# Optimization experiments

Hardware: AMD Instinct MI355X
Metric: run time of the kernel (lower is better)

## Reference

```python
import jax, jax.numpy as jnp
import numpy as np

B, T, C = 4, 2048, 1024
N_HEAD = 16
HEAD = C // N_HEAD  # 64


def _rope_tables(T, dim, base=10000.0):
    inv_freq = 1.0 / (base ** (jnp.arange(0, dim, 2, dtype=jnp.float32) / dim))
    t = jnp.arange(T, dtype=jnp.float32)
    freqs = jnp.einsum('i,j->ij', t, inv_freq)           # [T, dim/2]
    emb = jnp.concatenate([freqs, freqs], axis=-1)        # [T, dim]
    return jnp.cos(emb), jnp.sin(emb)                     # each [T, dim]


def _rotate_half(x):
    x1, x2 = x[..., : x.shape[-1] // 2], x[..., x.shape[-1] // 2:]
    return jnp.concatenate([-x2, x1], axis=-1)


def setup_inputs() -> dict:
    key = jax.random.key(0)
    ks = jax.random.split(key, 4)
    x = jax.random.normal(ks[0], (B, T, C), dtype=jnp.float32)
    w_attn = jax.random.normal(ks[1], (C, 3 * C), dtype=jnp.float32) * (1.0 / np.sqrt(C))
    b_attn = jnp.zeros((3 * C,), dtype=jnp.float32)
    w_proj = jax.random.normal(ks[2], (C, C), dtype=jnp.float32) * (1.0 / np.sqrt(C))
    b_proj = jnp.zeros((C,), dtype=jnp.float32)
    return {"x": x, "w_attn": w_attn, "b_attn": b_attn, "w_proj": w_proj, "b_proj": b_proj}


def reference(x, w_attn, b_attn, w_proj, b_proj):
    Bx, Tx, Cx = x.shape
    qkv = x @ w_attn + b_attn                             # [B,T,3C]
    q, k, v = jnp.split(qkv, 3, axis=-1)
    # [B,T,C] -> [B,H,T,hd]
    def to_heads(t):
        return t.reshape(Bx, Tx, N_HEAD, HEAD).transpose(0, 2, 1, 3)
    q, k, v = to_heads(q), to_heads(k), to_heads(v)
    cos, sin = _rope_tables(Tx, HEAD)                     # [T,hd]
    cos = cos[None, None, :, :]
    sin = sin[None, None, :, :]
    q = q * cos + _rotate_half(q) * sin
    k = k * cos + _rotate_half(k) * sin
    scale = 1.0 / np.sqrt(HEAD)
    att = jnp.einsum('bhqd,bhkd->bhqk', q, k) * scale     # [B,H,T,T]
    causal = jnp.tril(jnp.ones((Tx, Tx), dtype=bool))
    att = jnp.where(causal[None, None], att, -jnp.inf)
    att = jax.nn.softmax(att, axis=-1)
    y = jnp.einsum('bhqk,bhkd->bhqd', att, v)             # [B,H,T,hd]
    y = y.transpose(0, 2, 1, 3).reshape(Bx, Tx, Cx)
    return y @ w_proj + b_proj
```

## Files before the change

### kernel.cpp

```cpp
#include <hip/hip_runtime.h>

#define B_  4
#define T_  2048
#define C_  1024
#define NH_ 16
#define HD_ 64
#define BT_ (B_*T_)
#define N3C (3*C_)

typedef _Float16 f16;
typedef _Float16 half8 __attribute__((ext_vector_type(8)));
typedef _Float16 half4 __attribute__((ext_vector_type(4)));
typedef _Float16 half2v __attribute__((ext_vector_type(2)));
typedef float f32x4 __attribute__((ext_vector_type(4)));

__device__ __forceinline__ void gld16(const f16* g, f16* l) {
  __builtin_amdgcn_global_load_lds(
      (const __attribute__((address_space(1))) unsigned int*)g,
      (__attribute__((address_space(3))) unsigned int*)l, 16, 0, 0);
}

__device__ __forceinline__ float fast_exp2(float x) {
#if __has_builtin(__builtin_amdgcn_exp2f)
  return __builtin_amdgcn_exp2f(x);
#else
  return exp2f(x);
#endif
}

__device__ __forceinline__ half2v cvt_pk_f16(float a, float b) {
#if __has_builtin(__builtin_amdgcn_cvt_pkrtz)
  return __builtin_bit_cast(half2v, __builtin_amdgcn_cvt_pkrtz(a, b));
#else
  half2v r; r[0] = (f16)a; r[1] = (f16)b; return r;
#endif
}

__global__ __launch_bounds__(256) void prep(
    const float* __restrict__ X, f16* __restrict__ X16,
    const float* __restrict__ Wa, f16* __restrict__ Wta,
    const float* __restrict__ Wp, f16* __restrict__ Wtp,
    float2* __restrict__ cs)
{
  __shared__ float Ls[64][65];
  const int tid = threadIdx.x;
  const int blk = blockIdx.x;
  if (blk < 4096) {
    const int i = blk * 256 + tid;
    const float4 a = ((const float4*)X)[i * 2];
    const float4 b = ((const float4*)X)[i * 2 + 1];
    half8 hx;
    hx[0] = (f16)a.x; hx[1] = (f16)a.y; hx[2] = (f16)a.z; hx[3] = (f16)a.w;
    hx[4] = (f16)b.x; hx[5] = (f16)b.y; hx[6] = (f16)b.z; hx[7] = (f16)b.w;
    ((half8*)X16)[i] = hx;
    return;
  }
  if (blk >= 5120) {
    const int i = (blk - 5120) * 256 + tid;
    const int f = i & 31, t = i >> 5;
    const float inv = expf(-(2.0f * (float)f / 64.0f) * 9.210340371976184f);
    float sn, cn;
    sincosf((float)t * inv, &sn, &cn);
    cs[i] = make_float2(cn, sn);
    return;
  }
  const float* W; f16* Wt; int N, i2;
  if (blk < 4864) { W = Wa; Wt = Wta; N = N3C; i2 = blk - 4096; }
  else            { W = Wp; Wt = Wtp; N = C_;  i2 = blk - 4864; }
  const int nblk = N >> 6;
  const int n0 = (i2 % nblk) * 64, k0 = (i2 / nblk) * 64;
#pragma unroll
  for (int j = 0; j < 4; ++j) {
    const int idx = j * 256 + tid;
    const int r = idx >> 4, c = (idx & 15) * 4;
    const float4 w = *(const float4*)(W + (size_t)(k0 + r) * N + n0 + c);
    Ls[r][c + 0] = w.x; Ls[r][c + 1] = w.y; Ls[r][c + 2] = w.z; Ls[r][c + 3] = w.w;
  }
  __syncthreads();
#pragma unroll
  for (int j = 0; j < 2; ++j) {
    const int idx = j * 256 + tid;
    const int r = idx >> 3, c = (idx & 7) * 8;
    half8 hw;
#pragma unroll
    for (int u = 0; u < 8; ++u) hw[u] = (f16)Ls[c + u][r];
    *(half8*)(Wt + (size_t)(n0 + r) * C_ + k0 + c) = hw;
  }
}

__global__ __launch_bounds__(256) void gemm_qkv(
    const f16* __restrict__ A, const f16* __restrict__ Bt,
    const float* __restrict__ bias, const float2* __restrict__ cs,
    f16* __restrict__ Qo, f16* __restrict__ Ko, f16* __restrict__ Vt_g)
{
  __shared__ f16 S[16384];
  f16* As = S;
  f16* Bs = S + 8192;
  const int tid  = threadIdx.x;
  const int row0 = blockIdx.y * 128;
  const int col0 = blockIdx.x * 128;
  const int wave = tid >> 6, lane = tid & 63;
  const int l = lane & 15, quad = lane >> 4;
  const int wm = wave >> 1, wn = wave & 1;
  const int sr = tid >> 3;
  const int scs = ((tid & 7) ^ (sr & 7)) * 8;
  const int lq7 = l & 7;

  f32x4 acc[4][4];
#pragma unroll
  for (int mi = 0; mi < 4; ++mi)
#pragma unroll
    for (int ni = 0; ni < 4; ++ni) acc[mi][ni] = (f32x4)0.0f;

  for (int k0 = 0; k0 < C_; k0 += 64) {
    __syncthreads();
#pragma unroll
    for (int p = 0; p < 4; ++p) {
      const int r = p * 32 + sr;
      gld16(A  + (size_t)(row0 + r) * C_ + k0 + scs, &As[p * 2048 + tid * 8]);
      gld16(Bt + (size_t)(col0 + r) * C_ + k0 + scs, &Bs[p * 2048 + tid * 8]);
    }
    __syncthreads();

#pragma unroll
    for (int s = 0; s < 2; ++s) {
      half8 af[4], bf[4];
#pragma unroll
      for (int mi = 0; mi < 4; ++mi)
        af[mi] = *(const half8*)&As[(wm * 64 + mi * 16 + l) * 64 + ((((s << 2) | quad) ^ lq7) << 3)];
#pragma unroll
      for (int ni = 0; ni < 4; ++ni)
        bf[ni] = *(const half8*)&Bs[(wn * 64 + ni * 16 + l) * 64 + ((((s << 2) | quad) ^ lq7) << 3)];
#pragma unroll
      for (int mi = 0; mi < 4; ++mi)
#pragma unroll
        for (int ni = 0; ni < 4; ++ni)
          acc[mi][ni] = __builtin_amdgcn_mfma_f32_16x16x32_f16(af[mi], bf[ni], acc[mi][ni], 0, 0, 0);
    }
  }

  const int region = col0 >> 10;
  const int colw = col0 + wn * 64;
  const int bloc  = row0 >> 11;
  const int tbase = row0 & (T_ - 1);
  if (region < 2) {
    f16* dst = (region == 0) ? Qo : Ko;
    const float qs = (region == 0) ? 0.18033688f : 1.0f;
    __syncthreads();
#pragma unroll
    for (int mi = 0; mi < 4; ++mi) {
#pragma unroll
      for (int r = 0; r < 4; ++r) {
        const int t = wm * 64 + mi * 16 + quad * 4 + r;
        const int swz = ((t >> 2) & 3) << 3;
        const float2* csrow = cs + (tbase + t) * 32;
#pragma unroll
        for (int ni = 0; ni < 2; ++ni) {
          const int d = ni * 16 + l;
          const float2 c2 = csrow[d];
          const float x1 = acc[mi][ni][r]     + bias[colw + d];
          const float x2 = acc[mi][ni + 2][r] + bias[colw + d + 32];
          S[wn * 8192 + t * 64 + (d ^ swz)]        = (f16)((x1 * c2.x - x2 * c2.y) * qs);
          S[wn * 8192 + t * 64 + ((d + 32) ^ swz)] = (f16)((x2 * c2.x + x1 * c2.y) * qs);
        }
      }
    }
    __syncthreads();
#pragma unroll
    for (int j = 0; j < 8; ++j) {
      const int flat = j * 256 + tid;
      const int wnn  = flat >> 10;
      const int rem  = flat & 1023;
      const int t    = rem >> 3;
      const int d8   = rem & 7;
      const int swz  = (t >> 2) & 3;
      const half8 v  = *(const half8*)&S[wnn * 8192 + t * 64 + ((d8 ^ swz) << 3)];
      const int hh   = ((col0 + wnn * 64) & 1023) >> 6;
      *(half8*)(dst + ((size_t)(bloc * NH_ + hh) * T_ + tbase + t) * HD_ + d8 * 8) = v;
    }
  } else {
    __syncthreads();
#pragma unroll
    for (int mi = 0; mi < 4; ++mi) {
      const int t_loc = wm * 64 + mi * 16 + quad * 4;
#pragma unroll
      for (int ni = 0; ni < 4; ++ni) {
        const int d = ni * 16 + l;
        const float bs = bias[colw + d];
        half4 o;
#pragma unroll
        for (int r = 0; r < 4; ++r) o[r] = (f16)(acc[mi][ni][r] + bs);
        const int ts = t_loc ^ ((d & 15) << 3);
        *(half4*)&S[wn * 8192 + d * 128 + ts] = o;
      }
    }
    __syncthreads();
#pragma unroll
    for (int j = 0; j < 8; ++j) {
      const int flat = j * 256 + tid;
      const int buf  = flat >> 10;
      const int rem  = flat & 1023;
      const int d    = rem >> 4;
      const int tt   = (rem & 15) << 3;
      const half8 v  = *(const half8*)&S[buf * 8192 + d * 128 + (tt ^ ((d & 15) << 3))];
      const int hh   = ((col0 + buf * 64) & 1023) >> 6;
      *(half8*)(Vt_g + ((size_t)((bloc * NH_ + hh) * HD_ + d)) * T_ + tbase + tt) = v;
    }
  }
}

__global__ __launch_bounds__(256) void attn_mfma(
    const f16* __restrict__ Qg, const f16* __restrict__ Kg,
    const f16* __restrict__ Vt_g, f16* __restrict__ Y)
{
  __shared__ f16 Ks[2][64 * 64];
  __shared__ f16 Vt[2][64 * 64];
  const int tid  = threadIdx.x;
  const int w    = (blockIdx.x & 7) * 128 + (blockIdx.x >> 3);
  const int bh   = w >> 4;
  const int pr   = w & 15;
  const int b    = bh >> 4, h = bh & 15;
  const int wave = tid >> 6, lane = tid & 63;
  const int l    = lane & 15, quad = lane >> 4;
  const int lq7  = l & 7;
  const int r0   = tid >> 3, cc = tid & 7;

  const f16* kbase  = Kg   + (size_t)bh * T_ * HD_;
  const f16* vtbase = Vt_g + (size_t)bh * HD_ * T_;

  const int qts[2] = { 31 - pr, pr };

#pragma unroll 1
  for (int pass = 0; pass < 2; ++pass) {
    const int qt   = qts[pass];
    const int nkt  = qt + 1;
    const int qrow = qt * 64 + wave * 16 + l;

    half8 qf[2];
    {
      const f16* qp = Qg + ((size_t)bh * T_ + qrow) * HD_;
      qf[0] = *(const half8*)(qp + quad * 8);
      qf[1] = *(const half8*)(qp + 32 + quad * 8);
    }

    f32x4 O[4];
#pragma unroll
    for (int mi = 0; mi < 4; ++mi) O[mi] = (f32x4)0.0f;
    float l_run = 0.f;
    const f32x4 zz = (f32x4)0.0f;

    half8 hk[2], hv[2];
#pragma unroll
    for (int i = 0; i < 2; ++i) {
      const int r = i * 32 + r0;
      hk[i] = *(const half8*)(kbase + (size_t)r * HD_ + cc * 8);
      hv[i] = *(const half8*)(vtbase + (size_t)r * T_ + cc * 8);
    }

    if (pass == 1) __syncthreads();

    for (int kt = 0; kt < nkt; ++kt) {
      f16* KsB = Ks[kt & 1];
      f16* VtB = Vt[kt & 1];
#pragma unroll
      for (int i = 0; i < 2; ++i) {
        const int r = i * 32 + r0;
        const int cst = ((cc ^ (r & 7)) << 3);
        *(half8*)&KsB[r * 64 + cst] = hk[i];
        *(half8*)&VtB[r * 64 + cst] = hv[i];
      }
      __syncthreads();
      if (kt + 1 < nkt) {
#pragma unroll
        for (int i = 0; i < 2; ++i) {
          const int r = i * 32 + r0;
          hk[i] = *(const half8*)(kbase + (size_t)((kt + 1) * 64 + r) * HD_ + cc * 8);
          hv[i] = *(const half8*)(vtbase + (size_t)r * T_ + (kt + 1) * 64 + cc * 8);
        }
      }

      f32x4 St[4];
#pragma unroll
      for (int st = 0; st < 4; ++st) {
        const int row = st * 16 + l;
        const half8 af0 = *(const half8*)&KsB[row * 64 + (((quad) ^ lq7) << 3)];
        St[st] = __builtin_amdgcn_mfma_f32_16x16x32_f16(af0, qf[0], zz, 0, 0, 0);
        const half8 af1 = *(const half8*)&KsB[row * 64 + (((4 | quad) ^ lq7) << 3)];
        St[st] = __builtin_amdgcn_mfma_f32_16x16x32_f16(af1, qf[1], St[st], 0, 0, 0);
      }

      const bool domask = (kt == qt);
      const int k0 = kt * 64;
      half4 pf[4];
      float psum = 0.f;
#pragma unroll
      for (int st = 0; st < 4; ++st) {
        float pv[4];
#pragma unroll
        for (int r = 0; r < 4; ++r) {
          float x = St[st][r];
          if (domask) {
            const int key = k0 + st * 16 + quad * 4 + r;
            if (key > qrow) x = -1e9f;
          }
          const float ev = fast_exp2(x);
          pv[r] = ev;
          psum += ev;
        }
        const half2v lo = cvt_pk_f16(pv[0], pv[1]);
        const half2v hi = cvt_pk_f16(pv[2], pv[3]);
        pf[st][0] = lo[0]; pf[st][1] = lo[1];
        pf[st][2] = hi[0]; pf[st][3] = hi[1];
      }
      l_run += psum;

#pragma unroll
      for (int mi = 0; mi < 4; ++mi) {
        const int row = mi * 16 + l;
#pragma unroll
        for (int ki = 0; ki < 4; ++ki) {
          const int kch = (ki << 1) | (quad >> 1);
          const half4 vf = *(const half4*)&VtB[row * 64 + ((kch ^ lq7) << 3) + ((quad & 1) << 2)];
          O[mi] = __builtin_amdgcn_mfma_f32_16x16x16f16(vf, pf[ki], O[mi], 0, 0, 0);
        }
      }
    }

    float lt = l_run;
    lt += __shfl_xor(lt, 16);
    lt += __shfl_xor(lt, 32);
    const float inv = 1.0f / lt;
    f16* yp = Y + ((size_t)(b * T_) + qrow) * C_ + h * 64;
#pragma unroll
    for (int mi = 0; mi < 4; ++mi) {
      half4 o;
      o[0] = (f16)(O[mi][0] * inv); o[1] = (f16)(O[mi][1] * inv);
      o[2] = (f16)(O[mi][2] * inv); o[3] = (f16)(O[mi][3] * inv);
      *(half4*)(yp + mi * 16 + quad * 4) = o;
    }
  }
}

__global__ __launch_bounds__(256) void gemm_proj(
    const f16* __restrict__ A, const f16* __restrict__ Bt,
    const float* __restrict__ bias, float* __restrict__ Out)
{
  __shared__ f16 As[128 * 64];
  __shared__ f16 Bs[64 * 64];
  const int tid  = threadIdx.x;
  const int row0 = blockIdx.y * 128;
  const int col0 = blockIdx.x * 64;
  const int wave = tid >> 6, lane = tid & 63;
  const int l = lane & 15, quad = lane >> 4;
  const int wm = wave >> 1, wn = wave & 1;
  const int sr = tid >> 3;
  const int scs = ((tid & 7) ^ (sr & 7)) * 8;
  const int lq7 = l & 7;

  f32x4 acc[4][2];
#pragma unroll
  for (int mi = 0; mi < 4; ++mi)
#pragma unroll
    for (int ni = 0; ni < 2; ++ni) acc[mi][ni] = (f32x4)0.0f;

  for (int k0 = 0; k0 < C_; k0 += 64) {
    __syncthreads();
#pragma unroll
    for (int p = 0; p < 4; ++p) {
      const int r = p * 32 + sr;
      gld16(A + (size_t)(row0 + r) * C_ + k0 + scs, &As[p * 2048 + tid * 8]);
    }
#pragma unroll
    for (int p = 0; p < 2; ++p) {
      const int r = p * 32 + sr;
      gld16(Bt + (size_t)(col0 + r) * C_ + k0 + scs, &Bs[p * 2048 + tid * 8]);
    }
    __syncthreads();

#pragma unroll
    for (int s = 0; s < 2; ++s) {
      half8 af[4], bf[2];
#pragma unroll
      for (int mi = 0; mi < 4; ++mi)
        af[mi] = *(const half8*)&As[(wm * 64 + mi * 16 + l) * 64 + ((((s << 2) | quad) ^ lq7) << 3)];
#pragma unroll
      for (int ni = 0; ni < 2; ++ni)
        bf[ni] = *(const half8*)&Bs[(wn * 32 + ni * 16 + l) * 64 + ((((s << 2) | quad) ^ lq7) << 3)];
#pragma unroll
      for (int mi = 0; mi < 4; ++mi)
#pragma unroll
        for (int ni = 0; ni < 2; ++ni)
          acc[mi][ni] = __builtin_amdgcn_mfma_f32_16x16x32_f16(af[mi], bf[ni], acc[mi][ni], 0, 0, 0);
    }
  }

#pragma unroll
  for (int mi = 0; mi < 4; ++mi) {
#pragma unroll
    for (int ni = 0; ni < 2; ++ni) {
#pragma unroll
      for (int r = 0; r < 4; ++r) {
        const int gm = row0 + wm * 64 + mi * 16 + quad * 4 + r;
        const int n  = col0 + wn * 32 + ni * 16 + l;
        Out[(size_t)gm * C_ + n] = acc[mi][ni][r] + bias[n];
      }
    }
  }
}

extern "C" void kernel_launch(void* const* d_in, const int* in_sizes, int n_in,
                              void* d_out, int out_size, void* d_ws, size_t ws_size,
                              hipStream_t stream) {
  const float* x      = (const float*)d_in[0];
  const float* w_attn = (const float*)d_in[1];
  const float* b_attn = (const float*)d_in[2];
  const float* w_proj = (const float*)d_in[3];
  const float* b_proj = (const float*)d_in[4];
  float* out = (float*)d_out;

  const size_t elems = (size_t)BT_ * C_;
  f16* x16 = (f16*)d_ws;
  f16* wta = x16 + elems;
  f16* wtp = wta + (size_t)N3C * C_;
  f16* q   = wtp + (size_t)C_ * C_;
  f16* k   = q + elems;
  f16* vt  = k + elems;
  f16* y   = vt + elems;
  float2* cs = (float2*)(y + elems);

  prep<<<dim3(5376), 256, 0, stream>>>(x, x16, w_attn, wta, w_proj, wtp, cs);
  gemm_qkv<<<dim3(N3C / 128, BT_ / 128), 256, 0, stream>>>(x16, wta, b_attn, cs, q, k, vt);
  attn_mfma<<<dim3(1024), 256, 0, stream>>>(q, k, vt, y);
  gemm_proj<<<dim3(C_ / 64, BT_ / 128), 256, 0, stream>>>(y, wtp, b_proj, out);
}
```

Measured before the change: 259.3 us.

## Fuse x fp32-to-fp16 conversion into QKV GEMM and widen proj tile

The separate prep pass that converted x to fp16 is removed. The QKV GEMM now loads fp32 x directly, converts it in registers and writes it to shared memory, which saves one full-activation write and read. In exchange those A loads become synchronous register loads rather than async global-to-LDS loads, and each 128-column block re-reads the fp32 rows. The projection GEMM tile also widens from 128x64 to 128x128, giving more reuse per block but half as many blocks.

Result: slower. 275.2 us (+6.1%).

```diff
diff --git a/kernel.cpp b/kernel.cpp
--- a/kernel.cpp
+++ b/kernel.cpp
@@ -37,7 +37,6 @@
 }
 
 __global__ __launch_bounds__(256) void prep(
-    const float* __restrict__ X, f16* __restrict__ X16,
     const float* __restrict__ Wa, f16* __restrict__ Wta,
     const float* __restrict__ Wp, f16* __restrict__ Wtp,
     float2* __restrict__ cs)
@@ -45,18 +44,8 @@
   __shared__ float Ls[64][65];
   const int tid = threadIdx.x;
   const int blk = blockIdx.x;
-  if (blk < 4096) {
-    const int i = blk * 256 + tid;
-    const float4 a = ((const float4*)X)[i * 2];
-    const float4 b = ((const float4*)X)[i * 2 + 1];
-    half8 hx;
-    hx[0] = (f16)a.x; hx[1] = (f16)a.y; hx[2] = (f16)a.z; hx[3] = (f16)a.w;
-    hx[4] = (f16)b.x; hx[5] = (f16)b.y; hx[6] = (f16)b.z; hx[7] = (f16)b.w;
-    ((half8*)X16)[i] = hx;
-    return;
-  }
-  if (blk >= 5120) {
-    const int i = (blk - 5120) * 256 + tid;
+  if (blk >= 1024) {
+    const int i = (blk - 1024) * 256 + tid;
     const int f = i & 31, t = i >> 5;
     const float inv = expf(-(2.0f * (float)f / 64.0f) * 9.210340371976184f);
     float sn, cn;
@@ -65,8 +54,8 @@
     return;
   }
   const float* W; f16* Wt; int N, i2;
-  if (blk < 4864) { W = Wa; Wt = Wta; N = N3C; i2 = blk - 4096; }
-  else            { W = Wp; Wt = Wtp; N = C_;  i2 = blk - 4864; }
+  if (blk < 768) { W = Wa; Wt = Wta; N = N3C; i2 = blk; }
+  else           { W = Wp; Wt = Wtp; N = C_;  i2 = blk - 768; }
   const int nblk = N >> 6;
   const int n0 = (i2 % nblk) * 64, k0 = (i2 / nblk) * 64;
 #pragma unroll
@@ -89,7 +78,7 @@
 }
 
 __global__ __launch_bounds__(256) void gemm_qkv(
-    const f16* __restrict__ A, const f16* __restrict__ Bt,
+    const float* __restrict__ X, const f16* __restrict__ Bt,
     const float* __restrict__ bias, const float2* __restrict__ cs,
     f16* __restrict__ Qo, f16* __restrict__ Ko, f16* __restrict__ Vt_g)
 {
@@ -117,8 +106,27 @@
 #pragma unroll
     for (int p = 0; p < 4; ++p) {
       const int r = p * 32 + sr;
-      gld16(A  + (size_t)(row0 + r) * C_ + k0 + scs, &As[p * 2048 + tid * 8]);
       gld16(Bt + (size_t)(col0 + r) * C_ + k0 + scs, &Bs[p * 2048 + tid * 8]);
+    }
+#pragma unroll
+    for (int g = 0; g < 2; ++g) {
+      float4 fa[2][2];
+#pragma unroll
+      for (int pp = 0; pp < 2; ++pp) {
+        const int r = (g * 2 + pp) * 32 + sr;
+        const float* src = X + (size_t)(row0 + r) * C_ + k0 + scs;
+        fa[pp][0] = *(const float4*)(src);
+        fa[pp][1] = *(const float4*)(src + 4);
+      }
+#pragma unroll
+      for (int pp = 0; pp < 2; ++pp) {
+        half8 hx;
+        hx[0] = (f16)fa[pp][0].x; hx[1] = (f16)fa[pp][0].y;
+        hx[2] = (f16)fa[pp][0].z; hx[3] = (f16)fa[pp][0].w;
+        hx[4] = (f16)fa[pp][1].x; hx[5] = (f16)fa[pp][1].y;
+        hx[6] = (f16)fa[pp][1].z; hx[7] = (f16)fa[pp][1].w;
+        *(half8*)&As[(g * 2 + pp) * 2048 + tid * 8] = hx;
+      }
     }
     __syncthreads();
 
@@ -346,10 +354,10 @@
     const float* __restrict__ bias, float* __restrict__ Out)
 {
   __shared__ f16 As[128 * 64];
-  __shared__ f16 Bs[64 * 64];
+  __shared__ f16 Bs[128 * 64];
   const int tid  = threadIdx.x;
   const int row0 = blockIdx.y * 128;
-  const int col0 = blockIdx.x * 64;
+  const int col0 = blockIdx.x * 128;
   const int wave = tid >> 6, lane = tid & 63;
   const int l = lane & 15, quad = lane >> 4;
   const int wm = wave >> 1, wn = wave & 1;
@@ -357,39 +365,35 @@
   const int scs = ((tid & 7) ^ (sr & 7)) * 8;
   const int lq7 = l & 7;
 
-  f32x4 acc[4][2];
+  f32x4 acc[4][4];
 #pragma unroll
   for (int mi = 0; mi < 4; ++mi)
 #pragma unroll
-    for (int ni = 0; ni < 2; ++ni) acc[mi][ni] = (f32x4)0.0f;
+    for (int ni = 0; ni < 4; ++ni) acc[mi][ni] = (f32x4)0.0f;
 
   for (int k0 = 0; k0 < C_; k0 += 64) {
     __syncthreads();
 #pragma unroll
     for (int p = 0; p < 4; ++p) {
       const int r = p * 32 + sr;
-      gld16(A + (size_t)(row0 + r) * C_ + k0 + scs, &As[p * 2048 + tid * 8]);
-    }
-#pragma unroll
-    for (int p = 0; p < 2; ++p) {
-      const int r = p * 32 + sr;
+      gld16(A  + (size_t)(row0 + r) * C_ + k0 + scs, &As[p * 2048 + tid * 8]);
       gld16(Bt + (size_t)(col0 + r) * C_ + k0 + scs, &Bs[p * 2048 + tid * 8]);
     }
     __syncthreads();
 
 #pragma unroll
     for (int s = 0; s < 2; ++s) {
-      half8 af[4], bf[2];
+      half8 af[4], bf[4];
 #pragma unroll
       for (int mi = 0; mi < 4; ++mi)
         af[mi] = *(const half8*)&As[(wm * 64 + mi * 16 + l) * 64 + ((((s << 2) | quad) ^ lq7) << 3)];
 #pragma unroll
-      for (int ni = 0; ni < 2; ++ni)
-        bf[ni] = *(const half8*)&Bs[(wn * 32 + ni * 16 + l) * 64 + ((((s << 2) | quad) ^ lq7) << 3)];
+      for (int ni = 0; ni < 4; ++ni)
+        bf[ni] = *(const half8*)&Bs[(wn * 64 + ni * 16 + l) * 64 + ((((s << 2) | quad) ^ lq7) << 3)];
 #pragma unroll
       for (int mi = 0; mi < 4; ++mi)
 #pragma unroll
-        for (int ni = 0; ni < 2; ++ni)
+        for (int ni = 0; ni < 4; ++ni)
           acc[mi][ni] = __builtin_amdgcn_mfma_f32_16x16x32_f16(af[mi], bf[ni], acc[mi][ni], 0, 0, 0);
     }
   }
@@ -397,11 +401,11 @@
 #pragma unroll
   for (int mi = 0; mi < 4; ++mi) {
 #pragma unroll
-    for (int ni = 0; ni < 2; ++ni) {
+    for (int ni = 0; ni < 4; ++ni) {
 #pragma unroll
       for (int r = 0; r < 4; ++r) {
         const int gm = row0 + wm * 64 + mi * 16 + quad * 4 + r;
-        const int n  = col0 + wn * 32 + ni * 16 + l;
+        const int n  = col0 + wn * 64 + ni * 16 + l;
         Out[(size_t)gm * C_ + n] = acc[mi][ni][r] + bias[n];
       }
     }
@@ -419,8 +423,7 @@
   float* out = (float*)d_out;
 
   const size_t elems = (size_t)BT_ * C_;
-  f16* x16 = (f16*)d_ws;
-  f16* wta = x16 + elems;
+  f16* wta = (f16*)d_ws;
   f16* wtp = wta + (size_t)N3C * C_;
   f16* q   = wtp + (size_t)C_ * C_;
   f16* k   = q + elems;
@@ -428,8 +431,8 @@
   f16* y   = vt + elems;
   float2* cs = (float2*)(y + elems);
 
-  prep<<<dim3(5376), 256, 0, stream>>>(x, x16, w_attn, wta, w_proj, wtp, cs);
-  gemm_qkv<<<dim3(N3C / 128, BT_ / 128), 256, 0, stream>>>(x16, wta, b_attn, cs, q, k, vt);
+  prep<<<dim3(1280), 256, 0, stream>>>(w_attn, wta, w_proj, wtp, cs);
+  gemm_qkv<<<dim3(N3C / 128, BT_ / 128), 256, 0, stream>>>(x, wta, b_attn, cs, q, k, vt);
   attn_mfma<<<dim3(1024), 256, 0, stream>>>(q, k, vt, y);
-  gemm_proj<<<dim3(C_ / 64, BT_ / 128), 256, 0, stream>>>(y, wtp, b_proj, out);
-}
+  gemm_proj<<<dim3(C_ / 128, BT_ / 128), 256, 0, stream>>>(y, wtp, b_proj, out);
+}
```
